# Kernel optimization log

Hardware: AMD Instinct MI355X
Metric: run time of the kernel (lower is better)

## Reference

```python
import jax, jax.numpy as jnp
import numpy as np

D_MODEL = 256
SCALE = 1.0 / np.sqrt(D_MODEL).astype(np.float32)


def setup_inputs() -> dict:
    key = jax.random.key(0)
    ks = jax.random.split(key, 8)
    B, M, d = 32, 8192, D_MODEL
    lim = 1.0 / np.sqrt(d)  # torch Linear default init range
    inp = {
        "query": jax.random.normal(ks[0], (B, d), dtype=jnp.float32),
        "tokens": jax.random.normal(ks[1], (B, M, d), dtype=jnp.float32),
        "q_w": jax.random.uniform(ks[2], (d, d), jnp.float32, -lim, lim),
        "q_b": jax.random.uniform(ks[3], (d,), jnp.float32, -lim, lim),
        "k_w": jax.random.uniform(ks[4], (d, d), jnp.float32, -lim, lim),
        "k_b": jax.random.uniform(ks[5], (d,), jnp.float32, -lim, lim),
        "v_w": jax.random.uniform(ks[6], (d, d), jnp.float32, -lim, lim),
        "v_b": jax.random.uniform(ks[7], (d,), jnp.float32, -lim, lim),
    }
    return inp


def reference(query, tokens, q_w, q_b, k_w, k_b, v_w, v_b):
    # q: [B, d]; k, v: [B, M, d]  (torch Linear: x @ W.T + b)
    q = query @ q_w.T + q_b
    k = tokens @ k_w.T + k_b
    v = tokens @ v_w.T + v_b
    # single-query scores: [B, M]
    logits = jnp.einsum("bd,bmd->bm", q, k) * SCALE
    w = jax.nn.softmax(logits, axis=-1)
    # weighted sum over tokens -> [B, d]
    return jnp.einsum("bm,bmd->bd", w, v)
```

## Files before the change

### kernel.cpp

```cpp
#include <hip/hip_runtime.h>
#include <math.h>

#define BB 32
#define MM 8192
#define DD 256
#define SCALE 0.0625f
#define WPB 128
#define TPW (MM / WPB)
#define BLK_PER_B (WPB / 4)

using f4 = __attribute__((ext_vector_type(4))) float;

__global__ __launch_bounds__(256) void k_qr(
    const float* __restrict__ query, const float* __restrict__ q_w,
    const float* __restrict__ q_b, const float* __restrict__ k_w,
    float* __restrict__ r)
{
    const int b = blockIdx.x, tid = threadIdx.x;
    __shared__ float qv[DD];
    __shared__ float qp[DD];
    qv[tid] = query[b * DD + tid];
    __syncthreads();
    float acc = q_b[tid];
    const float* qwrow = q_w + (size_t)tid * DD;
    #pragma unroll 8
    for (int e = 0; e < DD; ++e) acc += qv[e] * qwrow[e];
    qp[tid] = acc;
    __syncthreads();
    float racc = 0.f;
    #pragma unroll 8
    for (int d = 0; d < DD; ++d) racc += qp[d] * k_w[d * DD + tid];
    r[b * DD + tid] = racc * SCALE;
}

__global__ __launch_bounds__(256) void k_flash(
    const float* __restrict__ tokens, const float* __restrict__ r,
    float* __restrict__ part_m, float* __restrict__ part_l,
    f4* __restrict__ part_u)
{
    const int b    = blockIdx.y;
    const int blk  = blockIdx.x;
    const int tid  = threadIdx.x;
    const int w    = tid >> 6;
    const int lane = tid & 63;
    const int wi   = blk * 4 + w;
    const int m0   = wi * TPW;

    const f4* r4 = (const f4*)(r + b * DD);
    const f4 rr  = r4[lane];

    const f4* tok = (const f4*)tokens + ((size_t)b * MM + m0) * (DD / 4) + lane;

    float mw = -INFINITY, lw = 0.f;
    f4 u = {0.f, 0.f, 0.f, 0.f};

    for (int t = 0; t < TPW; t += 8) {
        f4 x[8];
        #pragma unroll
        for (int j = 0; j < 8; ++j)
            x[j] = __builtin_nontemporal_load(tok + (size_t)(t + j) * (DD / 4));

        float p[8];
        #pragma unroll
        for (int j = 0; j < 8; ++j)
            p[j] = x[j].x * rr.x + x[j].y * rr.y + x[j].z * rr.z + x[j].w * rr.w;

        #pragma unroll
        for (int o = 32; o > 0; o >>= 1) {
            #pragma unroll
            for (int j = 0; j < 8; ++j)
                p[j] += __shfl_xor(p[j], o);
        }

        float m8 = p[0];
        #pragma unroll
        for (int j = 1; j < 8; ++j) m8 = fmaxf(m8, p[j]);

        if (m8 > mw) {
            const float alpha = __expf(mw - m8);
            mw = m8;
            lw *= alpha;
            u.x *= alpha; u.y *= alpha; u.z *= alpha; u.w *= alpha;
        }

        #pragma unroll
        for (int j = 0; j < 8; ++j) {
            const float wj = __expf(p[j] - mw);
            lw += wj;
            u.x += wj * x[j].x;
            u.y += wj * x[j].y;
            u.z += wj * x[j].z;
            u.w += wj * x[j].w;
        }
    }

    const int pi = b * WPB + wi;
    if (lane == 0) { part_m[pi] = mw; part_l[pi] = lw; }
    part_u[(size_t)pi * 64 + lane] = u;
}

__global__ __launch_bounds__(256) void k_combine(
    const float* __restrict__ part_m, const float* __restrict__ part_l,
    const float* __restrict__ part_u, const float* __restrict__ v_w,
    const float* __restrict__ v_b, float* __restrict__ out)
{
    const int b = blockIdx.x, tid = threadIdx.x;
    __shared__ float red[256];
    __shared__ float sf[WPB];
    __shared__ float su[DD];

    const float pm = (tid < WPB) ? part_m[b * WPB + tid] : -INFINITY;
    red[tid] = pm;
    __syncthreads();
    #pragma unroll
    for (int s = 128; s > 0; s >>= 1) {
        if (tid < s) red[tid] = fmaxf(red[tid], red[tid + s]);
        __syncthreads();
    }
    const float gm = red[0];
    __syncthreads();

    float lterm = 0.f;
    if (tid < WPB) {
        const float f = __expf(pm - gm);
        sf[tid] = f;
        lterm = part_l[b * WPB + tid] * f;
    }
    red[tid] = lterm;
    __syncthreads();
    #pragma unroll
    for (int s = 128; s > 0; s >>= 1) {
        if (tid < s) red[tid] += red[tid + s];
        __syncthreads();
    }
    const float l = red[0];

    float acc = 0.f;
    const float* pu = part_u + (size_t)b * WPB * DD;
    #pragma unroll 4
    for (int i = 0; i < WPB; ++i) acc += pu[i * DD + tid] * sf[i];
    su[tid] = acc / l;
    __syncthreads();

    float o = v_b[tid];
    const float* vrow = v_w + (size_t)tid * DD;
    #pragma unroll 8
    for (int e = 0; e < DD; ++e) o += su[e] * vrow[e];
    out[b * DD + tid] = o;
}

extern "C" void kernel_launch(void* const* d_in, const int* in_sizes, int n_in,
                              void* d_out, int out_size, void* d_ws, size_t ws_size,
                              hipStream_t stream) {
    const float* query  = (const float*)d_in[0];
    const float* tokens = (const float*)d_in[1];
    const float* q_w    = (const float*)d_in[2];
    const float* q_b    = (const float*)d_in[3];
    const float* k_w    = (const float*)d_in[4];
    const float* v_w    = (const float*)d_in[6];
    const float* v_b    = (const float*)d_in[7];
    float* out = (float*)d_out;

    float* ws     = (float*)d_ws;
    float* r      = ws;
    float* part_m = r + BB * DD;
    float* part_l = part_m + BB * WPB;
    float* part_u = part_l + BB * WPB;

    k_qr<<<dim3(BB), dim3(256), 0, stream>>>(query, q_w, q_b, k_w, r);
    k_flash<<<dim3(BLK_PER_B, BB), dim3(256), 0, stream>>>(
        tokens, r, part_m, part_l, (f4*)part_u);
    k_combine<<<dim3(BB), dim3(256), 0, stream>>>(
        part_m, part_l, part_u, v_w, v_b, out);
}
```

Baseline: 399.5 us.

## Split wavefront into four 16-lane token groups with register prefetch

Each wavefront now processes four tokens at once, with 16 lanes per token each holding 64 floats. This cuts the cross-lane dot-product reduction from 6 shuffles per token to 4 shuffles shared across the four tokens. A software-prefetched next tile is added for load overlap. Each lane group keeps its own online-softmax state, and the groups are merged by shuffles at the end. In exchange it adds per-token exp work and rescaling, and fewer loads are in flight per iteration (4 versus 8).

```diff
diff --git a/kernel.cpp b/kernel.cpp
--- a/kernel.cpp
+++ b/kernel.cpp
@@ -43,60 +43,92 @@
     const int tid  = threadIdx.x;
     const int w    = tid >> 6;
     const int lane = tid & 63;
+    const int g    = lane & 15;
+    const int tg   = lane >> 4;
     const int wi   = blk * 4 + w;
     const int m0   = wi * TPW;
 
     const f4* r4 = (const f4*)(r + b * DD);
-    const f4 rr  = r4[lane];
-
-    const f4* tok = (const f4*)tokens + ((size_t)b * MM + m0) * (DD / 4) + lane;
+    f4 rr[4];
+    #pragma unroll
+    for (int c = 0; c < 4; ++c) rr[c] = r4[16 * c + g];
+
+    const f4* tok = (const f4*)tokens + ((size_t)b * MM + m0) * (DD / 4)
+                  + (size_t)tg * (DD / 4) + g;
 
     float mw = -INFINITY, lw = 0.f;
-    f4 u = {0.f, 0.f, 0.f, 0.f};
-
-    for (int t = 0; t < TPW; t += 8) {
-        f4 x[8];
+    f4 u[4] = {{0,0,0,0},{0,0,0,0},{0,0,0,0},{0,0,0,0}};
+
+    f4 xn[4];
+    #pragma unroll
+    for (int c = 0; c < 4; ++c)
+        xn[c] = __builtin_nontemporal_load(tok + 16 * c);
+
+    const int NIT = TPW / 4;
+    for (int it = 0; it < NIT; ++it) {
+        f4 x[4];
         #pragma unroll
-        for (int j = 0; j < 8; ++j)
-            x[j] = __builtin_nontemporal_load(tok + (size_t)(t + j) * (DD / 4));
-
-        float p[8];
+        for (int c = 0; c < 4; ++c) x[c] = xn[c];
+
+        if (it + 1 < NIT) {
+            const f4* nxt = tok + (size_t)(it + 1) * 4 * (DD / 4);
+            #pragma unroll
+            for (int c = 0; c < 4; ++c)
+                xn[c] = __builtin_nontemporal_load(nxt + 16 * c);
+        }
+
+        float s0 = x[0].x*rr[0].x + x[0].y*rr[0].y + x[0].z*rr[0].z + x[0].w*rr[0].w;
+        float s1 = x[1].x*rr[1].x + x[1].y*rr[1].y + x[1].z*rr[1].z + x[1].w*rr[1].w;
+        float s2 = x[2].x*rr[2].x + x[2].y*rr[2].y + x[2].z*rr[2].z + x[2].w*rr[2].w;
+        float s3 = x[3].x*rr[3].x + x[3].y*rr[3].y + x[3].z*rr[3].z + x[3].w*rr[3].w;
+        float p  = (s0 + s1) + (s2 + s3);
+
+        p += __shfl_xor(p, 1);
+        p += __shfl_xor(p, 2);
+        p += __shfl_xor(p, 4);
+        p += __shfl_xor(p, 8);
+
+        const float newm  = fmaxf(mw, p);
+        const float alpha = __expf(mw - newm);
+        const float wj    = __expf(p  - newm);
+        mw = newm;
+        lw = lw * alpha + wj;
         #pragma unroll
-        for (int j = 0; j < 8; ++j)
-            p[j] = x[j].x * rr.x + x[j].y * rr.y + x[j].z * rr.z + x[j].w * rr.w;
-
-        #pragma unroll
-        for (int o = 32; o > 0; o >>= 1) {
-            #pragma unroll
-            for (int j = 0; j < 8; ++j)
-                p[j] += __shfl_xor(p[j], o);
+        for (int c = 0; c < 4; ++c) {
+            u[c].x = u[c].x * alpha + wj * x[c].x;
+            u[c].y = u[c].y * alpha + wj * x[c].y;
+            u[c].z = u[c].z * alpha + wj * x[c].z;
+            u[c].w = u[c].w * alpha + wj * x[c].w;
         }
-
-        float m8 = p[0];
-        #pragma unroll
-        for (int j = 1; j < 8; ++j) m8 = fmaxf(m8, p[j]);
-
-        if (m8 > mw) {
-            const float alpha = __expf(mw - m8);
-            mw = m8;
-            lw *= alpha;
-            u.x *= alpha; u.y *= alpha; u.z *= alpha; u.w *= alpha;
-        }
-
-        #pragma unroll
-        for (int j = 0; j < 8; ++j) {
-            const float wj = __expf(p[j] - mw);
-            lw += wj;
-            u.x += wj * x[j].x;
-            u.y += wj * x[j].y;
-            u.z += wj * x[j].z;
-            u.w += wj * x[j].w;
-        }
+    }
+
+    float gm = mw;
+    gm = fmaxf(gm, __shfl_xor(gm, 16));
+    gm = fmaxf(gm, __shfl_xor(gm, 32));
+    const float beta = __expf(mw - gm);
+    float L = lw * beta;
+    L += __shfl_xor(L, 16);
+    L += __shfl_xor(L, 32);
+    #pragma unroll
+    for (int c = 0; c < 4; ++c) {
+        u[c].x *= beta; u[c].y *= beta; u[c].z *= beta; u[c].w *= beta;
+        u[c].x += __shfl_xor(u[c].x, 16);
+        u[c].y += __shfl_xor(u[c].y, 16);
+        u[c].z += __shfl_xor(u[c].z, 16);
+        u[c].w += __shfl_xor(u[c].w, 16);
+        u[c].x += __shfl_xor(u[c].x, 32);
+        u[c].y += __shfl_xor(u[c].y, 32);
+        u[c].z += __shfl_xor(u[c].z, 32);
+        u[c].w += __shfl_xor(u[c].w, 32);
     }
 
     const int pi = b * WPB + wi;
-    if (lane == 0) { part_m[pi] = mw; part_l[pi] = lw; }
-    part_u[(size_t)pi * 64 + lane] = u;
+    if (lane == 0) { part_m[pi] = gm; part_l[pi] = L; }
+    f4 val = u[0];
+    val = (tg == 1) ? u[1] : val;
+    val = (tg == 2) ? u[2] : val;
+    val = (tg == 3) ? u[3] : val;
+    part_u[(size_t)pi * 64 + lane] = val;
 }
 
 __global__ __launch_bounds__(256) void k_combine(
```

Measured after the change: 398.0 us. Within noise of the previous version (-0.4%).
